# Performance work log

Hardware: AMD Instinct MI355X
Metric: run time of the kernel (lower is better)

The kernel has to match this reference:

```python
import jax, jax.numpy as jnp
import numpy as np

B, S, D, DK, DV = 8, 2048, 256, 128, 128

def setup_inputs() -> dict:
    key = jax.random.key(0)
    ks = jax.random.split(key, 9)
    return {
        "x_q": jax.random.normal(ks[0], (B, S, D), jnp.float32),
        "x_k": jax.random.normal(ks[1], (B, S, D), jnp.float32),
        "x_v": jax.random.normal(ks[2], (B, S, D), jnp.float32),
        "Wq": jax.random.normal(ks[3], (D, DK), jnp.float32) * (1.0 / np.sqrt(D)),
        "bq": jax.random.normal(ks[4], (DK,), jnp.float32) * 0.02,
        "Wk": jax.random.normal(ks[5], (D, DK), jnp.float32) * (1.0 / np.sqrt(D)),
        "bk": jax.random.normal(ks[6], (DK,), jnp.float32) * 0.02,
        "Wv": jax.random.normal(ks[7], (D, DV), jnp.float32) * (1.0 / np.sqrt(D)),
        "bv": jax.random.normal(ks[8], (DV,), jnp.float32) * 0.02,
    }

def reference(x_q, x_k, x_v, Wq, bq, Wk, bk, Wv, bv):
    # Dense projections: [B,S,D] @ [D,dk] + bias
    q = jnp.einsum("bsd,dk->bsk", x_q, Wq) + bq
    k = jnp.einsum("bsd,dk->bsk", x_k, Wk) + bk
    v = jnp.einsum("bsd,dv->bsv", x_v, Wv) + bv
    scale = 1.0 / np.sqrt(Wq.shape[1]).astype(np.float32)  # 1/sqrt(d_k)
    scores = jnp.einsum("bqk,bsk->bqs", q, k) * scale       # [B,S,S]
    attn = jax.nn.softmax(scores, axis=-1)
    return jnp.einsum("bqs,bsv->bqv", attn, v)               # [B,S,d_v]
```

## Files before the change

kernel.cpp:

```cpp
#include <hip/hip_runtime.h>
#include <stdint.h>

typedef float    f32x4 __attribute__((ext_vector_type(4)));
typedef _Float16 f16x8 __attribute__((ext_vector_type(8)));
typedef _Float16 f16x4 __attribute__((ext_vector_type(4)));
typedef unsigned int u32x4 __attribute__((ext_vector_type(4)));

#define SPLIT 4

__device__ __forceinline__ f32x4 mfma16(f16x8 a, f16x8 b, f32x4 c) {
    return __builtin_amdgcn_mfma_f32_16x16x32_f16(a, b, c, 0, 0, 0);
}

__global__ __launch_bounds__(256) void prep_weights(
    const float* __restrict__ Wq, const float* __restrict__ Wk,
    const float* __restrict__ Wv, _Float16* __restrict__ wt) {
    __shared__ float Ls[64 * 65];
    const int bx = blockIdx.x;
    const int w  = bx >> 3, t = bx & 7;
    const int k0 = (t >> 1) * 64, n0 = (t & 1) * 64;
    const float* W = (w == 0) ? Wq : (w == 1) ? Wk : Wv;
    const int tid = threadIdx.x;
    #pragma unroll
    for (int i = 0; i < 16; i++) {
        int idx = i * 256 + tid;
        int r = idx >> 6, c = idx & 63;
        Ls[r * 65 + c] = W[(k0 + r) * 128 + n0 + c];
    }
    __syncthreads();
    #pragma unroll
    for (int i = 0; i < 16; i++) {
        int idx = i * 256 + tid;
        int r2 = idx >> 6, c2 = idx & 63;
        wt[w * 32768 + (n0 + r2) * 256 + k0 + c2] = (_Float16)Ls[c2 * 65 + r2];
    }
}

__global__ __launch_bounds__(256) void proj_kernel(
    const float* __restrict__ xq, const float* __restrict__ xk,
    const float* __restrict__ xv, const _Float16* __restrict__ wt,
    const float* __restrict__ bq, const float* __restrict__ bk,
    const float* __restrict__ bv,
    _Float16* __restrict__ qo, _Float16* __restrict__ ko,
    _Float16* __restrict__ vt)
{
    const int mode = blockIdx.y;
    const int row0 = blockIdx.x * 64;
    const float*    X    = mode == 0 ? xq : mode == 1 ? xk : xv;
    const float*    bias = mode == 0 ? bq : mode == 1 ? bk : bv;
    const _Float16* W    = wt + mode * 32768;

    __shared__ __align__(16) _Float16 Xs[64 * 40];
    __shared__ __align__(16) _Float16 Ws[128 * 40];

    const int tid  = threadIdx.x;
    const int wave = tid >> 6, lane = tid & 63;
    const int ln   = lane & 15, qd = lane >> 4;

    f32x4 acc[8];
    #pragma unroll
    for (int i = 0; i < 8; i++) acc[i] = (f32x4){0.f, 0.f, 0.f, 0.f};

    for (int kk = 0; kk < 8; kk++) {
        const int k0 = kk * 32;
        __syncthreads();
        #pragma unroll
        for (int i = tid; i < 512; i += 256) {
            int r = i >> 3, c = i & 7;
            f32x4 d = *(const f32x4*)(X + (size_t)(row0 + r) * 256 + k0 + c * 4);
            f16x4 h;
            h[0] = (_Float16)d[0]; h[1] = (_Float16)d[1];
            h[2] = (_Float16)d[2]; h[3] = (_Float16)d[3];
            *(f16x4*)&Xs[r * 40 + c * 4] = h;
        }
        #pragma unroll
        for (int i = tid; i < 512; i += 256) {
            int n = i >> 2, c = i & 3;
            *(u32x4*)&Ws[n * 40 + c * 8] =
                *(const u32x4*)(W + n * 256 + k0 + c * 8);
        }
        __syncthreads();
        f16x8 af = *(const f16x8*)&Xs[(wave * 16 + ln) * 40 + qd * 8];
        #pragma unroll
        for (int nt = 0; nt < 8; nt++) {
            f16x8 bf = *(const f16x8*)&Ws[(nt * 16 + ln) * 40 + qd * 8];
            acc[nt] = mfma16(af, bf, acc[nt]);
        }
    }

    const float SC = 0.08838834764831845f * 1.4426950408889634f;
    #pragma unroll
    for (int nt = 0; nt < 8; nt++) {
        int col = nt * 16 + ln;
        float bb = bias[col];
        #pragma unroll
        for (int r = 0; r < 4; r++) {
            int row = row0 + wave * 16 + qd * 4 + r;
            float val = acc[nt][r] + bb;
            if (mode == 0) {
                qo[(size_t)row * 128 + col] = (_Float16)(val * SC);
            } else if (mode == 1) {
                ko[(size_t)row * 128 + col] = (_Float16)val;
            } else {
                int b = row >> 11, s = row & 2047;
                vt[((size_t)(b * 128 + col)) * 2048 + s] = (_Float16)val;
            }
        }
    }
}

__global__ __launch_bounds__(256) void attn_kernel(
    const _Float16* __restrict__ qp, const _Float16* __restrict__ kp,
    const _Float16* __restrict__ vtp, _Float16* __restrict__ opart,
    float2* __restrict__ ml)
{
    const int b  = blockIdx.y;
    const int z  = blockIdx.z;
    const int q0 = blockIdx.x * 64;
    const int tid  = threadIdx.x;
    const int wave = tid >> 6, lane = tid & 63;
    const int ln   = lane & 15, qd = lane >> 4;

    __shared__ __align__(16) _Float16 Ks[64 * 136];
    __shared__ __align__(16) _Float16 Vs[128 * 72];
    __shared__ __align__(16) _Float16 Ps[4 * 16 * 72];

    const _Float16* qrow =
        qp + (size_t)(b * 2048 + q0 + wave * 16 + ln) * 128 + qd * 8;
    f16x8 qf[4];
    #pragma unroll
    for (int c = 0; c < 4; c++) qf[c] = *(const f16x8*)(qrow + c * 32);

    f32x4 o[8];
    #pragma unroll
    for (int i = 0; i < 8; i++) o[i] = (f32x4){0.f, 0.f, 0.f, 0.f};
    float m_run[4] = {-1e30f, -1e30f, -1e30f, -1e30f};
    float l_run[4] = {0.f, 0.f, 0.f, 0.f};

    const _Float16* kbase = kp + (size_t)b * 2048 * 128;
    const _Float16* vbase = vtp + (size_t)b * 128 * 2048;

    for (int kt = z * 8; kt < z * 8 + 8; kt++) {
        __syncthreads();
        const _Float16* ks = kbase + kt * 64 * 128;
        #pragma unroll
        for (int i = tid; i < 1024; i += 256) {
            int r = i >> 4, c = i & 15;
            *(u32x4*)&Ks[r * 136 + c * 8] = *(const u32x4*)(ks + r * 128 + c * 8);
        }
        const _Float16* vs = vbase + kt * 64;
        #pragma unroll
        for (int i = tid; i < 1024; i += 256) {
            int r = i >> 3, c = i & 7;
            *(u32x4*)&Vs[r * 72 + c * 8] =
                *(const u32x4*)(vs + (size_t)r * 2048 + c * 8);
        }
        __syncthreads();

        f32x4 sc[4];
        #pragma unroll
        for (int st = 0; st < 4; st++) {
            sc[st] = (f32x4){0.f, 0.f, 0.f, 0.f};
            int base = (st * 16 + ln) * 136 + qd * 8;
            #pragma unroll
            for (int c = 0; c < 4; c++) {
                f16x8 kf = *(const f16x8*)&Ks[base + c * 32];
                sc[st] = mfma16(qf[c], kf, sc[st]);
            }
        }

        float mnew[4], alpha[4];
        #pragma unroll
        for (int r = 0; r < 4; r++) {
            float t = fmaxf(fmaxf(sc[0][r], sc[1][r]), fmaxf(sc[2][r], sc[3][r]));
            t = fmaxf(t, __shfl_xor(t, 1));
            t = fmaxf(t, __shfl_xor(t, 2));
            t = fmaxf(t, __shfl_xor(t, 4));
            t = fmaxf(t, __shfl_xor(t, 8));
            mnew[r]  = fmaxf(m_run[r], t);
            alpha[r] = exp2f(m_run[r] - mnew[r]);
        }
        #pragma unroll
        for (int st = 0; st < 4; st++)
            #pragma unroll
            for (int r = 0; r < 4; r++) {
                float p = exp2f(sc[st][r] - mnew[r]);
                sc[st][r] = p;
                Ps[wave * 1152 + (qd * 4 + r) * 72 + st * 16 + ln] = (_Float16)p;
            }
        #pragma unroll
        for (int r = 0; r < 4; r++) {
            float s = sc[0][r] + sc[1][r] + sc[2][r] + sc[3][r];
            s += __shfl_xor(s, 1); s += __shfl_xor(s, 2);
            s += __shfl_xor(s, 4); s += __shfl_xor(s, 8);
            l_run[r] = l_run[r] * alpha[r] + s;
            m_run[r] = mnew[r];
        }
        #pragma unroll
        for (int dt = 0; dt < 8; dt++)
            #pragma unroll
            for (int r = 0; r < 4; r++) o[dt][r] *= alpha[r];

        #pragma unroll
        for (int c = 0; c < 2; c++) {
            f16x8 pf = *(const f16x8*)&Ps[wave * 1152 + ln * 72 + c * 32 + qd * 8];
            #pragma unroll
            for (int dt = 0; dt < 8; dt++) {
                f16x8 vf = *(const f16x8*)&Vs[(dt * 16 + ln) * 72 + c * 32 + qd * 8];
                o[dt] = mfma16(pf, vf, o[dt]);
            }
        }
    }

    const size_t prow = (size_t)(z * 8 + b) * 2048 + q0 + wave * 16;
    _Float16* op = opart + (prow + qd * 4) * 128;
    #pragma unroll
    for (int dt = 0; dt < 8; dt++)
        #pragma unroll
        for (int r = 0; r < 4; r++)
            op[(size_t)r * 128 + dt * 16 + ln] = (_Float16)o[dt][r];
    if (ln == 0) {
        #pragma unroll
        for (int r = 0; r < 4; r++) {
            float2 v; v.x = m_run[r]; v.y = l_run[r];
            ml[prow + qd * 4 + r] = v;
        }
    }
}

__global__ __launch_bounds__(256) void merge_kernel(
    const _Float16* __restrict__ opart, const float2* __restrict__ ml,
    float* __restrict__ out)
{
    const int t = threadIdx.x;
    const int r = t >> 4, cg = t & 15;
    const size_t row = (size_t)blockIdx.x * 16 + r;

    float m[SPLIT], l[SPLIT], w[SPLIT];
    float M = -1e30f;
    #pragma unroll
    for (int zi = 0; zi < SPLIT; zi++) {
        float2 p = ml[(size_t)zi * 16384 + row];
        m[zi] = p.x; l[zi] = p.y; M = fmaxf(M, p.x);
    }
    float L = 0.f;
    #pragma unroll
    for (int zi = 0; zi < SPLIT; zi++) { w[zi] = exp2f(m[zi] - M); L += w[zi] * l[zi]; }
    const float inv = 1.0f / L;

    float acc[8] = {0.f, 0.f, 0.f, 0.f, 0.f, 0.f, 0.f, 0.f};
    #pragma unroll
    for (int zi = 0; zi < SPLIT; zi++) {
        f16x8 v = *(const f16x8*)&opart[((size_t)zi * 16384 + row) * 128 + cg * 8];
        #pragma unroll
        for (int j = 0; j < 8; j++) acc[j] += w[zi] * (float)v[j];
    }
    float* op = out + row * 128 + cg * 8;
    f32x4 lo = (f32x4){acc[0] * inv, acc[1] * inv, acc[2] * inv, acc[3] * inv};
    f32x4 hi = (f32x4){acc[4] * inv, acc[5] * inv, acc[6] * inv, acc[7] * inv};
    *(f32x4*)op = lo;
    *(f32x4*)(op + 4) = hi;
}

extern "C" void kernel_launch(void* const* d_in, const int* in_sizes, int n_in,
                              void* d_out, int out_size, void* d_ws, size_t ws_size,
                              hipStream_t stream) {
    const float* xq = (const float*)d_in[0];
    const float* xk = (const float*)d_in[1];
    const float* xv = (const float*)d_in[2];
    const float* Wq = (const float*)d_in[3];
    const float* bq = (const float*)d_in[4];
    const float* Wk = (const float*)d_in[5];
    const float* bk = (const float*)d_in[6];
    const float* Wv = (const float*)d_in[7];
    const float* bv = (const float*)d_in[8];
    float* out = (float*)d_out;

    char* ws = (char*)d_ws;
    _Float16* wt    = (_Float16*)ws;
    _Float16* qo    = (_Float16*)(ws + 196608);
    _Float16* ko    = (_Float16*)(ws + 196608 + 4194304);
    _Float16* vt    = (_Float16*)(ws + 196608 + 2 * 4194304);
    _Float16* opart = (_Float16*)(ws + 196608 + 3 * 4194304);
    float2*   ml    = (float2*)  (ws + 196608 + 3 * 4194304 + 16777216);

    hipLaunchKernelGGL(prep_weights, dim3(24), dim3(256), 0, stream,
                       Wq, Wk, Wv, wt);
    hipLaunchKernelGGL(proj_kernel, dim3(256, 3), dim3(256), 0, stream,
                       xq, xk, xv, wt, bq, bk, bv, qo, ko, vt);
    hipLaunchKernelGGL(attn_kernel, dim3(32, 8, SPLIT), dim3(256), 0, stream,
                       qo, ko, vt, opart, ml);
    hipLaunchKernelGGL(merge_kernel, dim3(1024), dim3(256), 0, stream,
                       opart, ml, out);
}
```

Measured before the change: 189.7 us.

## Load projection operands directly, add V transpose kernel, enlarge attention tiles

The projection kernel now loads X and the fp16 weights straight from global memory into MFMA fragments, with no LDS staging and no barriers. It writes V row-major to a scratch buffer that aliases opart, and a new tiled transpose kernel produces the V-transposed layout. This replaces the old scattered strided stores. The attention kernel now uses 512-thread blocks covering 128 queries, so each K/V tile loaded into LDS serves twice as many query rows. The cost is an extra kernel launch and higher per-block register and LDS pressure.

```diff
diff --git a/kernel.cpp b/kernel.cpp
--- a/kernel.cpp
+++ b/kernel.cpp
@@ -42,48 +42,38 @@
     const float* __restrict__ bq, const float* __restrict__ bk,
     const float* __restrict__ bv,
     _Float16* __restrict__ qo, _Float16* __restrict__ ko,
-    _Float16* __restrict__ vt)
+    _Float16* __restrict__ vtmp)
 {
     const int mode = blockIdx.y;
-    const int row0 = blockIdx.x * 64;
     const float*    X    = mode == 0 ? xq : mode == 1 ? xk : xv;
     const float*    bias = mode == 0 ? bq : mode == 1 ? bk : bv;
     const _Float16* W    = wt + mode * 32768;
-
-    __shared__ __align__(16) _Float16 Xs[64 * 40];
-    __shared__ __align__(16) _Float16 Ws[128 * 40];
+    _Float16*       Y    = mode == 0 ? qo : mode == 1 ? ko : vtmp;
 
     const int tid  = threadIdx.x;
     const int wave = tid >> 6, lane = tid & 63;
     const int ln   = lane & 15, qd = lane >> 4;
+    const int row0 = blockIdx.x * 64 + wave * 16;
+
+    const float*    xrow = X + (size_t)(row0 + ln) * 256 + qd * 8;
+    const _Float16* wb   = W + ln * 256 + qd * 8;
 
     f32x4 acc[8];
     #pragma unroll
     for (int i = 0; i < 8; i++) acc[i] = (f32x4){0.f, 0.f, 0.f, 0.f};
 
+    #pragma unroll
     for (int kk = 0; kk < 8; kk++) {
-        const int k0 = kk * 32;
-        __syncthreads();
-        #pragma unroll
-        for (int i = tid; i < 512; i += 256) {
-            int r = i >> 3, c = i & 7;
-            f32x4 d = *(const f32x4*)(X + (size_t)(row0 + r) * 256 + k0 + c * 4);
-            f16x4 h;
-            h[0] = (_Float16)d[0]; h[1] = (_Float16)d[1];
-            h[2] = (_Float16)d[2]; h[3] = (_Float16)d[3];
-            *(f16x4*)&Xs[r * 40 + c * 4] = h;
-        }
-        #pragma unroll
-        for (int i = tid; i < 512; i += 256) {
-            int n = i >> 2, c = i & 3;
-            *(u32x4*)&Ws[n * 40 + c * 8] =
-                *(const u32x4*)(W + n * 256 + k0 + c * 8);
-        }
-        __syncthreads();
-        f16x8 af = *(const f16x8*)&Xs[(wave * 16 + ln) * 40 + qd * 8];
+        f32x4 a0 = *(const f32x4*)(xrow + kk * 32);
+        f32x4 a1 = *(const f32x4*)(xrow + kk * 32 + 4);
+        f16x8 af;
+        af[0] = (_Float16)a0[0]; af[1] = (_Float16)a0[1];
+        af[2] = (_Float16)a0[2]; af[3] = (_Float16)a0[3];
+        af[4] = (_Float16)a1[0]; af[5] = (_Float16)a1[1];
+        af[6] = (_Float16)a1[2]; af[7] = (_Float16)a1[3];
         #pragma unroll
         for (int nt = 0; nt < 8; nt++) {
-            f16x8 bf = *(const f16x8*)&Ws[(nt * 16 + ln) * 40 + qd * 8];
+            f16x8 bf = *(const f16x8*)(wb + nt * 4096 + kk * 32);
             acc[nt] = mfma16(af, bf, acc[nt]);
         }
     }
@@ -95,35 +85,56 @@
         float bb = bias[col];
         #pragma unroll
         for (int r = 0; r < 4; r++) {
-            int row = row0 + wave * 16 + qd * 4 + r;
+            int orow = row0 + qd * 4 + r;
             float val = acc[nt][r] + bb;
-            if (mode == 0) {
-                qo[(size_t)row * 128 + col] = (_Float16)(val * SC);
-            } else if (mode == 1) {
-                ko[(size_t)row * 128 + col] = (_Float16)val;
-            } else {
-                int b = row >> 11, s = row & 2047;
-                vt[((size_t)(b * 128 + col)) * 2048 + s] = (_Float16)val;
-            }
-        }
-    }
-}
-
-__global__ __launch_bounds__(256) void attn_kernel(
+            if (mode == 0) val *= SC;
+            Y[(size_t)orow * 128 + col] = (_Float16)val;
+        }
+    }
+}
+
+__global__ __launch_bounds__(256) void transpose_v(
+    const _Float16* __restrict__ vtmp, _Float16* __restrict__ vt)
+{
+    __shared__ __align__(16) _Float16 Ls[64 * 72];
+    const int b  = blockIdx.z;
+    const int s0 = blockIdx.x * 64;
+    const int d0 = blockIdx.y * 64;
+    const int tid = threadIdx.x;
+    #pragma unroll
+    for (int i = 0; i < 2; i++) {
+        int idx = i * 256 + tid;
+        int r = idx >> 3, c = (idx & 7) * 8;
+        *(f16x8*)&Ls[r * 72 + c] =
+            *(const f16x8*)(vtmp + (size_t)(b * 2048 + s0 + r) * 128 + d0 + c);
+    }
+    __syncthreads();
+    #pragma unroll
+    for (int i = 0; i < 2; i++) {
+        int idx = i * 256 + tid;
+        int dr = idx >> 3, sc8 = (idx & 7) * 8;
+        f16x8 o;
+        #pragma unroll
+        for (int j = 0; j < 8; j++) o[j] = Ls[(sc8 + j) * 72 + dr];
+        *(f16x8*)(vt + (size_t)(b * 128 + d0 + dr) * 2048 + s0 + sc8) = o;
+    }
+}
+
+__global__ __launch_bounds__(512, 4) void attn_kernel(
     const _Float16* __restrict__ qp, const _Float16* __restrict__ kp,
     const _Float16* __restrict__ vtp, _Float16* __restrict__ opart,
     float2* __restrict__ ml)
 {
     const int b  = blockIdx.y;
     const int z  = blockIdx.z;
-    const int q0 = blockIdx.x * 64;
+    const int q0 = blockIdx.x * 128;
     const int tid  = threadIdx.x;
     const int wave = tid >> 6, lane = tid & 63;
     const int ln   = lane & 15, qd = lane >> 4;
 
     __shared__ __align__(16) _Float16 Ks[64 * 136];
     __shared__ __align__(16) _Float16 Vs[128 * 72];
-    __shared__ __align__(16) _Float16 Ps[4 * 16 * 72];
+    __shared__ __align__(16) _Float16 Ps[8 * 16 * 72];
 
     const _Float16* qrow =
         qp + (size_t)(b * 2048 + q0 + wave * 16 + ln) * 128 + qd * 8;
@@ -144,13 +155,13 @@
         __syncthreads();
         const _Float16* ks = kbase + kt * 64 * 128;
         #pragma unroll
-        for (int i = tid; i < 1024; i += 256) {
+        for (int i = tid; i < 1024; i += 512) {
             int r = i >> 4, c = i & 15;
             *(u32x4*)&Ks[r * 136 + c * 8] = *(const u32x4*)(ks + r * 128 + c * 8);
         }
         const _Float16* vs = vbase + kt * 64;
         #pragma unroll
-        for (int i = tid; i < 1024; i += 256) {
+        for (int i = tid; i < 1024; i += 512) {
             int r = i >> 3, c = i & 7;
             *(u32x4*)&Vs[r * 72 + c * 8] =
                 *(const u32x4*)(vs + (size_t)r * 2048 + c * 8);
@@ -282,13 +293,16 @@
     _Float16* ko    = (_Float16*)(ws + 196608 + 4194304);
     _Float16* vt    = (_Float16*)(ws + 196608 + 2 * 4194304);
     _Float16* opart = (_Float16*)(ws + 196608 + 3 * 4194304);
+    _Float16* vtmp  = opart;
     float2*   ml    = (float2*)  (ws + 196608 + 3 * 4194304 + 16777216);
 
     hipLaunchKernelGGL(prep_weights, dim3(24), dim3(256), 0, stream,
                        Wq, Wk, Wv, wt);
     hipLaunchKernelGGL(proj_kernel, dim3(256, 3), dim3(256), 0, stream,
-                       xq, xk, xv, wt, bq, bk, bv, qo, ko, vt);
-    hipLaunchKernelGGL(attn_kernel, dim3(32, 8, SPLIT), dim3(256), 0, stream,
+                       xq, xk, xv, wt, bq, bk, bv, qo, ko, vtmp);
+    hipLaunchKernelGGL(transpose_v, dim3(32, 2, 8), dim3(256), 0, stream,
+                       vtmp, vt);
+    hipLaunchKernelGGL(attn_kernel, dim3(16, 8, SPLIT), dim3(512), 0, stream,
                        qo, ko, vt, opart, ml);
     hipLaunchKernelGGL(merge_kernel, dim3(1024), dim3(256), 0, stream,
                        opart, ml, out);
```

New measurement: 175.3 us. 7.6% less time.
